# Kernel optimization log

Measured on AMD Instinct MI355X. Metric: run time of the kernel, lower is better.

Reference implementation:

```python
import jax, jax.numpy as jnp
import numpy as np
from jax import lax

K = 7  # kernel_size
PAD = K // 2


def _feature_difference(t):
    # t: [B, C, H, W] -> normalized census-style local differences [B, K*K, H, W]
    intensity = t.mean(axis=1, keepdims=True)  # [B,1,H,W]
    # Equivalent to conv2d with the identity (eye) kernel in the torch module:
    # channel k gathers the neighbor at offset (k//K, k%K) with zero padding.
    patches = lax.conv_general_dilated_patches(
        intensity, filter_shape=(K, K), window_strides=(1, 1),
        padding=[(PAD, PAD), (PAD, PAD)])  # [B, K*K, H, W]
    local_diff = patches - intensity
    return local_diff / jnp.sqrt(0.81 + local_diff * local_diff)


def setup_inputs() -> dict:
    key = jax.random.key(0)
    kx, ky = jax.random.split(key)
    B, C, H, W = 8, 3, 320, 1024
    x = jax.random.uniform(kx, (B, C, H, W), dtype=jnp.float32)
    y = jax.random.uniform(ky, (B, C, H, W), dtype=jnp.float32)
    return {"x": x, "y": y}


def reference(x, y):
    diff_x = _feature_difference(x)
    diff_y = _feature_difference(y)
    diff_total = diff_x - lax.stop_gradient(diff_y)  # .detach() on y branch
    d2 = diff_total * diff_total
    dist = (d2 / (0.1 + d2)).mean(axis=1, keepdims=True)  # [B,1,H,W]
    b, c, h, w = x.shape
    # valid-region mask: ones in the interior, zeros in the PAD-wide border
    mask = jnp.zeros((b, 1, h, w), dtype=x.dtype)
    mask = mask.at[:, :, PAD:h - PAD, PAD:w - PAD].set(1.0)
    return (dist * mask).mean()
```

## Files before the change

### kernel.cpp

```cpp
#include <hip/hip_runtime.h>

typedef float f32x2 __attribute__((ext_vector_type(2)));
typedef float f32x4 __attribute__((ext_vector_type(4)));

#define PAD 3
#define HH 320
#define WW 1024
#define BB 8
#define TH 32
#define TW 64
#define HALO_H (TH + 2*PAD)
#define LDS_W  72
#define NF4    (LDS_W/4)
#define NPOS   (HALO_H * NF4)
#define RPW 8

#define NIN ((HH - 2*PAD) * (WW - 2*PAD))
#define OUT_SCALE (1.0 / (49.0 * (double)BB * (double)HH * (double)WW))
#define C0 ((float)(48.0 * (double)BB * (double)NIN * OUT_SCALE))
#define NEG_SCALE ((float)(-0.1 * OUT_SCALE))

#define KEEP(v) asm("" : "+v"(v))

__device__ __forceinline__ f32x2 mk2(float a, float b) { f32x2 r; r.x = a; r.y = b; return r; }
__device__ __forceinline__ f32x2 sp2(float a)          { f32x2 r; r.x = a; r.y = a; return r; }
__device__ __forceinline__ f32x2 fma2(f32x2 a, f32x2 b, f32x2 c) {
    return __builtin_elementwise_fma(a, b, c);
}

__device__ __forceinline__ void pair2(f32x2 nx, f32x2 ny, f32x2 cx2, f32x2 cy2,
                                      f32x2 w2, float& acc)
{
    f32x2 dx  = nx - cx2;
    f32x2 dy  = ny - cy2;
    f32x2 dx2 = dx * dx;
    f32x2 dy2 = dy * dy;
    f32x2 ax  = dx2 + sp2(0.81f);
    f32x2 ay  = dy2 + sp2(0.81f);
    f32x2 P   = ax * ay;
    f32x2 s   = mk2(__builtin_amdgcn_rsqf(P.x), __builtin_amdgcn_rsqf(P.y));
    f32x2 A   = fma2(dx2, ay, dy2 * ax);
    f32x2 h   = dx * dy;
    f32x2 inner = fma2(s, A, h * sp2(-2.0f));
    f32x2 t2  = s * inner;
    f32x2 den = t2 + sp2(0.1f);
    float ip    = __builtin_amdgcn_rcpf(den.x * den.y);
    float cross = fmaf(w2.x, den.y, w2.y * den.x);
    acc = fmaf(ip, cross, acc);
}

__global__ __launch_bounds__(256, 4) void ternary_loss_kernel(
    const float* __restrict__ x, const float* __restrict__ y,
    float* __restrict__ out)
{
    __shared__ __align__(16) float sIx[HALO_H][LDS_W];
    __shared__ __align__(16) float sIy[HALO_H][LDS_W];
    __shared__ float wave_sums[4];

    const int tile_j = blockIdx.x * TW;
    const int tile_i = blockIdx.y * TH;
    const int b      = blockIdx.z;
    const int tx  = threadIdx.x;
    const int wv  = threadIdx.y;
    const int tid = wv * 64 + tx;

    const size_t PLANE = (size_t)HH * WW;
    const float* xb = x + (size_t)b * 3 * PLANE;
    const float* yb = y + (size_t)b * 3 * PLANE;

    for (int p = tid; p < NPOS; p += 256) {
        int r  = p / NF4;
        int c4 = p - r * NF4;
        int gi  = tile_i - PAD + r;
        int gj0 = tile_j - 4 + 4 * c4;
        f32x4 vx = {0.0f, 0.0f, 0.0f, 0.0f};
        f32x4 vy = {0.0f, 0.0f, 0.0f, 0.0f};
        if ((unsigned)gi < (unsigned)HH && (unsigned)gj0 < (unsigned)WW) {
            const float* px = xb + (size_t)gi * WW + gj0;
            f32x4 a0 = *(const f32x4*)(px);
            f32x4 a1 = *(const f32x4*)(px + PLANE);
            f32x4 a2 = *(const f32x4*)(px + 2 * PLANE);
            vx = (a0 + a1 + a2) * (1.0f / 3.0f);
            const float* py = yb + (size_t)gi * WW + gj0;
            f32x4 b0 = *(const f32x4*)(py);
            f32x4 b1 = *(const f32x4*)(py + PLANE);
            f32x4 b2 = *(const f32x4*)(py + 2 * PLANE);
            vy = (b0 + b1 + b2) * (1.0f / 3.0f);
        }
        *(f32x4*)&sIx[r][4 * c4] = vx;
        *(f32x4*)&sIy[r][4 * c4] = vy;
    }
    __syncthreads();

    const int gj = tile_j + tx;
    float cO[7];
    #pragma unroll
    for (int d = 0; d < 7; ++d) {
        int nj = gj + d - 3;
        cO[d] = (nj >= PAD && nj < WW - PAD) ? 1.0f : 0.0f;
    }
    const f32x2 cP0  = mk2(cO[0], cO[1]);
    const f32x2 cP1  = mk2(cO[2], cO[3]);
    const f32x2 cP2  = mk2(cO[4], cO[5]);
    const f32x2 cP3  = sp2(cO[6]);

    const int li0 = wv * RPW;

    float wx[4][7], wy[4][7];
    #pragma unroll
    for (int r = 0; r < 3; ++r) {
        #pragma unroll
        for (int d = 0; d < 7; ++d) {
            float a = sIx[li0 + 3 + r][tx + 1 + d]; KEEP(a); wx[r][d] = a;
            float c = sIy[li0 + 3 + r][tx + 1 + d]; KEEP(c); wy[r][d] = c;
        }
    }

    float acc = 0.0f;

    #pragma unroll 1
    for (int io = 0; io < RPW / 4; ++io) {
        #pragma unroll
        for (int iu = 0; iu < 4; ++iu) {
            const int li = li0 + io * 4 + iu;
            const int gi = tile_i + li;
            const int snew = (iu + 3) & 3;
            #pragma unroll
            for (int d = 0; d < 7; ++d) {
                float a = sIx[li + 6][tx + 1 + d]; KEEP(a); wx[snew][d] = a;
                float c = sIy[li + 6][tx + 1 + d]; KEEP(c); wy[snew][d] = c;
            }

            float rin[4];
            #pragma unroll
            for (int di = 0; di < 4; ++di) {
                int ni = gi + di;
                rin[di] = (ni >= PAD && ni < HH - PAD) ? 1.0f : 0.0f;
            }
            const float mc  = rin[0] * cO[3];
            const f32x2 mc2 = sp2(mc);

            const int s0 = iu & 3;
            const f32x2 cx2 = sp2(wx[s0][3]);
            const f32x2 cy2 = sp2(wy[s0][3]);

            pair2(mk2(wx[s0][4], wx[s0][5]), mk2(wy[s0][4], wy[s0][5]),
                  cx2, cy2, fma2(sp2(rin[0]), cP2, mc2), acc);

            #pragma unroll
            for (int di = 1; di <= 3; ++di) {
                const int s = (iu + di) & 3;
                const f32x2 rin2 = sp2(rin[di]);
                pair2(mk2(wx[s][0], wx[s][1]), mk2(wy[s][0], wy[s][1]),
                      cx2, cy2, fma2(rin2, cP0, mc2), acc);
                pair2(mk2(wx[s][2], wx[s][3]), mk2(wy[s][2], wy[s][3]),
                      cx2, cy2, fma2(rin2, cP1, mc2), acc);
                pair2(mk2(wx[s][4], wx[s][5]), mk2(wy[s][4], wy[s][5]),
                      cx2, cy2, fma2(rin2, cP2, mc2), acc);
            }

            {
                const int s1 = (iu + 1) & 3;
                const int s2 = (iu + 2) & 3;
                const int s3 = (iu + 3) & 3;
                pair2(mk2(wx[s0][6], wx[s1][6]), mk2(wy[s0][6], wy[s1][6]),
                      cx2, cy2, fma2(mk2(rin[0], rin[1]), cP3, mc2), acc);
                pair2(mk2(wx[s2][6], wx[s3][6]), mk2(wy[s2][6], wy[s3][6]),
                      cx2, cy2, fma2(mk2(rin[2], rin[3]), cP3, mc2), acc);
            }
        }
    }

    #pragma unroll
    for (int off = 32; off > 0; off >>= 1)
        acc += __shfl_down(acc, off, 64);
    if (tx == 0) wave_sums[wv] = acc;
    __syncthreads();
    if (tid == 0) {
        float total = (wave_sums[0] + wave_sums[1] + wave_sums[2] + wave_sums[3]) * NEG_SCALE;
        if (blockIdx.x == 0 && blockIdx.y == 0 && blockIdx.z == 0)
            total += C0;
        atomicAdd(out, total);
    }
}

extern "C" void kernel_launch(void* const* d_in, const int* in_sizes, int n_in,
                              void* d_out, int out_size, void* d_ws, size_t ws_size,
                              hipStream_t stream) {
    const float* x = (const float*)d_in[0];
    const float* y = (const float*)d_in[1];
    float* out = (float*)d_out;

    hipMemsetAsync(out, 0, sizeof(float), stream);

    dim3 grid(WW / TW, HH / TH, BB);
    dim3 block(64, 4, 1);
    ternary_loss_kernel<<<grid, block, 0, stream>>>(x, y, out);
}
```

Measured before the change: 120.6 us.

## Specialize interior tiles without masks and use 8 waves per block

Adds a templated fast path for tiles that lie fully inside the valid region. There the per-pair mask weights are all one, so the cross term reduces to den.x+den.y and the total is scaled by 2. The block also grows from 4 to 8 waves, each handling 4 rows instead of 8, to raise parallelism and spread the halo-load work. Code size rises because two specializations are instantiated, and per-wave work is smaller relative to the register-window setup.

```diff
diff --git a/kernel.cpp b/kernel.cpp
--- a/kernel.cpp
+++ b/kernel.cpp
@@ -13,7 +13,9 @@
 #define LDS_W  72
 #define NF4    (LDS_W/4)
 #define NPOS   (HALO_H * NF4)
-#define RPW 8
+#define RPW 4
+#define NWAVES 8
+#define NTHREADS (NWAVES * 64)
 
 #define NIN ((HH - 2*PAD) * (WW - 2*PAD))
 #define OUT_SCALE (1.0 / (49.0 * (double)BB * (double)HH * (double)WW))
@@ -28,6 +30,7 @@
     return __builtin_elementwise_fma(a, b, c);
 }
 
+template<bool INTERIOR>
 __device__ __forceinline__ void pair2(f32x2 nx, f32x2 ny, f32x2 cx2, f32x2 cy2,
                                       f32x2 w2, float& acc)
 {
@@ -45,17 +48,108 @@
     f32x2 t2  = s * inner;
     f32x2 den = t2 + sp2(0.1f);
     float ip    = __builtin_amdgcn_rcpf(den.x * den.y);
-    float cross = fmaf(w2.x, den.y, w2.y * den.x);
+    float cross;
+    if constexpr (INTERIOR) cross = den.x + den.y;
+    else                    cross = fmaf(w2.x, den.y, w2.y * den.x);
     acc = fmaf(ip, cross, acc);
 }
 
-__global__ __launch_bounds__(256, 4) void ternary_loss_kernel(
+template<bool INTERIOR>
+__device__ __forceinline__ float compute_rows(
+    const float (&sIx)[HALO_H][LDS_W], const float (&sIy)[HALO_H][LDS_W],
+    int tile_i, int tile_j, int tx, int wv)
+{
+    float cO[7] = {};
+    f32x2 cP0 = {}, cP1 = {}, cP2 = {}, cP3 = {};
+    if constexpr (!INTERIOR) {
+        const int gj = tile_j + tx;
+        #pragma unroll
+        for (int d = 0; d < 7; ++d) {
+            int nj = gj + d - 3;
+            cO[d] = (nj >= PAD && nj < WW - PAD) ? 1.0f : 0.0f;
+        }
+        cP0 = mk2(cO[0], cO[1]);
+        cP1 = mk2(cO[2], cO[3]);
+        cP2 = mk2(cO[4], cO[5]);
+        cP3 = sp2(cO[6]);
+    }
+
+    const int li0 = wv * RPW;
+
+    float wx[4][7], wy[4][7];
+    #pragma unroll
+    for (int r = 0; r < 3; ++r) {
+        #pragma unroll
+        for (int d = 0; d < 7; ++d) {
+            float a = sIx[li0 + 3 + r][tx + 1 + d]; KEEP(a); wx[r][d] = a;
+            float c = sIy[li0 + 3 + r][tx + 1 + d]; KEEP(c); wy[r][d] = c;
+        }
+    }
+
+    float acc = 0.0f;
+
+    #pragma unroll
+    for (int iu = 0; iu < RPW; ++iu) {
+        const int li = li0 + iu;
+        const int gi = tile_i + li;
+        const int snew = (iu + 3) & 3;
+        #pragma unroll
+        for (int d = 0; d < 7; ++d) {
+            float a = sIx[li + 6][tx + 1 + d]; KEEP(a); wx[snew][d] = a;
+            float c = sIy[li + 6][tx + 1 + d]; KEEP(c); wy[snew][d] = c;
+        }
+
+        float rin[4] = {};
+        f32x2 mc2 = {};
+        if constexpr (!INTERIOR) {
+            #pragma unroll
+            for (int di = 0; di < 4; ++di) {
+                int ni = gi + di;
+                rin[di] = (ni >= PAD && ni < HH - PAD) ? 1.0f : 0.0f;
+            }
+            mc2 = sp2(rin[0] * cO[3]);
+        }
+
+        const int s0 = iu & 3;
+        const f32x2 cx2 = sp2(wx[s0][3]);
+        const f32x2 cy2 = sp2(wy[s0][3]);
+
+        pair2<INTERIOR>(mk2(wx[s0][4], wx[s0][5]), mk2(wy[s0][4], wy[s0][5]),
+              cx2, cy2, INTERIOR ? sp2(0.0f) : fma2(sp2(rin[0]), cP2, mc2), acc);
+
+        #pragma unroll
+        for (int di = 1; di <= 3; ++di) {
+            const int s = (iu + di) & 3;
+            const f32x2 rin2 = sp2(rin[di]);
+            pair2<INTERIOR>(mk2(wx[s][0], wx[s][1]), mk2(wy[s][0], wy[s][1]),
+                  cx2, cy2, INTERIOR ? sp2(0.0f) : fma2(rin2, cP0, mc2), acc);
+            pair2<INTERIOR>(mk2(wx[s][2], wx[s][3]), mk2(wy[s][2], wy[s][3]),
+                  cx2, cy2, INTERIOR ? sp2(0.0f) : fma2(rin2, cP1, mc2), acc);
+            pair2<INTERIOR>(mk2(wx[s][4], wx[s][5]), mk2(wy[s][4], wy[s][5]),
+                  cx2, cy2, INTERIOR ? sp2(0.0f) : fma2(rin2, cP2, mc2), acc);
+        }
+
+        {
+            const int s1 = (iu + 1) & 3;
+            const int s2 = (iu + 2) & 3;
+            const int s3 = (iu + 3) & 3;
+            pair2<INTERIOR>(mk2(wx[s0][6], wx[s1][6]), mk2(wy[s0][6], wy[s1][6]),
+                  cx2, cy2, INTERIOR ? sp2(0.0f) : fma2(mk2(rin[0], rin[1]), cP3, mc2), acc);
+            pair2<INTERIOR>(mk2(wx[s2][6], wx[s3][6]), mk2(wy[s2][6], wy[s3][6]),
+                  cx2, cy2, INTERIOR ? sp2(0.0f) : fma2(mk2(rin[2], rin[3]), cP3, mc2), acc);
+        }
+    }
+
+    return acc;
+}
+
+__global__ __launch_bounds__(NTHREADS, 8) void ternary_loss_kernel(
     const float* __restrict__ x, const float* __restrict__ y,
     float* __restrict__ out)
 {
     __shared__ __align__(16) float sIx[HALO_H][LDS_W];
     __shared__ __align__(16) float sIy[HALO_H][LDS_W];
-    __shared__ float wave_sums[4];
+    __shared__ float wave_sums[NWAVES];
 
     const int tile_j = blockIdx.x * TW;
     const int tile_i = blockIdx.y * TH;
@@ -68,7 +162,7 @@
     const float* xb = x + (size_t)b * 3 * PLANE;
     const float* yb = y + (size_t)b * 3 * PLANE;
 
-    for (int p = tid; p < NPOS; p += 256) {
+    for (int p = tid; p < NPOS; p += NTHREADS) {
         int r  = p / NF4;
         int c4 = p - r * NF4;
         int gi  = tile_i - PAD + r;
@@ -92,84 +186,12 @@
     }
     __syncthreads();
 
-    const int gj = tile_j + tx;
-    float cO[7];
-    #pragma unroll
-    for (int d = 0; d < 7; ++d) {
-        int nj = gj + d - 3;
-        cO[d] = (nj >= PAD && nj < WW - PAD) ? 1.0f : 0.0f;
-    }
-    const f32x2 cP0  = mk2(cO[0], cO[1]);
-    const f32x2 cP1  = mk2(cO[2], cO[3]);
-    const f32x2 cP2  = mk2(cO[4], cO[5]);
-    const f32x2 cP3  = sp2(cO[6]);
-
-    const int li0 = wv * RPW;
-
-    float wx[4][7], wy[4][7];
-    #pragma unroll
-    for (int r = 0; r < 3; ++r) {
-        #pragma unroll
-        for (int d = 0; d < 7; ++d) {
-            float a = sIx[li0 + 3 + r][tx + 1 + d]; KEEP(a); wx[r][d] = a;
-            float c = sIy[li0 + 3 + r][tx + 1 + d]; KEEP(c); wy[r][d] = c;
-        }
-    }
-
-    float acc = 0.0f;
-
-    #pragma unroll 1
-    for (int io = 0; io < RPW / 4; ++io) {
-        #pragma unroll
-        for (int iu = 0; iu < 4; ++iu) {
-            const int li = li0 + io * 4 + iu;
-            const int gi = tile_i + li;
-            const int snew = (iu + 3) & 3;
-            #pragma unroll
-            for (int d = 0; d < 7; ++d) {
-                float a = sIx[li + 6][tx + 1 + d]; KEEP(a); wx[snew][d] = a;
-                float c = sIy[li + 6][tx + 1 + d]; KEEP(c); wy[snew][d] = c;
-            }
-
-            float rin[4];
-            #pragma unroll
-            for (int di = 0; di < 4; ++di) {
-                int ni = gi + di;
-                rin[di] = (ni >= PAD && ni < HH - PAD) ? 1.0f : 0.0f;
-            }
-            const float mc  = rin[0] * cO[3];
-            const f32x2 mc2 = sp2(mc);
-
-            const int s0 = iu & 3;
-            const f32x2 cx2 = sp2(wx[s0][3]);
-            const f32x2 cy2 = sp2(wy[s0][3]);
-
-            pair2(mk2(wx[s0][4], wx[s0][5]), mk2(wy[s0][4], wy[s0][5]),
-                  cx2, cy2, fma2(sp2(rin[0]), cP2, mc2), acc);
-
-            #pragma unroll
-            for (int di = 1; di <= 3; ++di) {
-                const int s = (iu + di) & 3;
-                const f32x2 rin2 = sp2(rin[di]);
-                pair2(mk2(wx[s][0], wx[s][1]), mk2(wy[s][0], wy[s][1]),
-                      cx2, cy2, fma2(rin2, cP0, mc2), acc);
-                pair2(mk2(wx[s][2], wx[s][3]), mk2(wy[s][2], wy[s][3]),
-                      cx2, cy2, fma2(rin2, cP1, mc2), acc);
-                pair2(mk2(wx[s][4], wx[s][5]), mk2(wy[s][4], wy[s][5]),
-                      cx2, cy2, fma2(rin2, cP2, mc2), acc);
-            }
-
-            {
-                const int s1 = (iu + 1) & 3;
-                const int s2 = (iu + 2) & 3;
-                const int s3 = (iu + 3) & 3;
-                pair2(mk2(wx[s0][6], wx[s1][6]), mk2(wy[s0][6], wy[s1][6]),
-                      cx2, cy2, fma2(mk2(rin[0], rin[1]), cP3, mc2), acc);
-                pair2(mk2(wx[s2][6], wx[s3][6]), mk2(wy[s2][6], wy[s3][6]),
-                      cx2, cy2, fma2(mk2(rin[2], rin[3]), cP3, mc2), acc);
-            }
-        }
-    }
+    const bool interior = (tile_i >= PAD) && (tile_i + TH + PAD <= HH - PAD)
+                       && (tile_j >= 2*PAD) && (tile_j + TW + PAD <= WW - PAD);
+
+    float acc;
+    if (interior) acc = 2.0f * compute_rows<true >(sIx, sIy, tile_i, tile_j, tx, wv);
+    else          acc =        compute_rows<false>(sIx, sIy, tile_i, tile_j, tx, wv);
 
     #pragma unroll
     for (int off = 32; off > 0; off >>= 1)
@@ -177,7 +199,10 @@
     if (tx == 0) wave_sums[wv] = acc;
     __syncthreads();
     if (tid == 0) {
-        float total = (wave_sums[0] + wave_sums[1] + wave_sums[2] + wave_sums[3]) * NEG_SCALE;
+        float total = 0.0f;
+        #pragma unroll
+        for (int w = 0; w < NWAVES; ++w) total += wave_sums[w];
+        total *= NEG_SCALE;
         if (blockIdx.x == 0 && blockIdx.y == 0 && blockIdx.z == 0)
             total += C0;
         atomicAdd(out, total);
@@ -194,6 +219,6 @@
     hipMemsetAsync(out, 0, sizeof(float), stream);
 
     dim3 grid(WW / TW, HH / TH, BB);
-    dim3 block(64, 4, 1);
+    dim3 block(64, NWAVES, 1);
     ternary_loss_kernel<<<grid, block, 0, stream>>>(x, y, out);
 }
```

Measured after the change: 147.1 us. 1.22x slower.
